# Kernel tuning notes

Measured on AMD Instinct MI355X. Metric: run time of the kernel, lower is better.

Reference implementation:

```python
import jax, jax.numpy as jnp
from jax import lax
import numpy as np

T, INPUT, RES, OUT = 4096, 64, 4096, 32
SPECTRAL_RADIUS, CONNECTIVITY = 0.9, 0.3


def setup_inputs() -> dict:
    key = jax.random.key(0)
    k_in, k_w, k_mask, k_x, k_out = jax.random.split(key, 5)
    inputs = jax.random.normal(k_x, (T, INPUT), dtype=jnp.float32)
    # W_in, W ~ U(-1, 1), as in (rand - 0.5) * 2
    W_in = jax.random.uniform(k_in, (RES, INPUT), minval=-1.0, maxval=1.0, dtype=jnp.float32)
    W = jax.random.uniform(k_w, (RES, RES), minval=-1.0, maxval=1.0, dtype=jnp.float32)
    mask = (jax.random.uniform(k_mask, (RES, RES)) < CONNECTIVITY).astype(jnp.float32)
    W = W * mask
    # rescale to spectral radius (done once at init; numpy eig on host)
    max_eig = np.max(np.abs(np.linalg.eigvals(np.asarray(W))))
    W = W / jnp.float32(max_eig / SPECTRAL_RADIUS)
    # trained readout (stand-in for pinv-solved W_out)
    W_out = jax.random.normal(k_out, (RES, OUT), dtype=jnp.float32) * 0.05
    return {"inputs": inputs, "W_in": W_in, "W": W, "W_out": W_out}


def reference(inputs, W_in, W, W_out):
    # X[:, 0] = 0; X[:, t] = tanh(W_in @ inputs[t] + W @ X[:, t-1]) for t >= 1
    u = inputs @ W_in.T  # [T, RES] precomputed input projections

    def step(x_prev, u_t):
        x_t = jnp.tanh(u_t + W @ x_prev)
        return x_t, x_t

    x0 = jnp.zeros((RES,), dtype=inputs.dtype)
    _, xs = lax.scan(step, x0, u[1:])  # [T-1, RES]
    X = jnp.concatenate([x0[None, :], xs], axis=0)  # [T, RES] == original X.T
    return X @ W_out  # [T, OUT]
```

## Files before the change

kernel.cpp:

```cpp
#include <hip/hip_runtime.h>

#define T_STEPS 4096
#define RES     4096
#define NIN     64
#define NOUT    32
#define NWG     256
#define TPB     512

typedef unsigned long long ull;

__device__ __forceinline__ bool rdy(ull q) {
    return (__uint_as_float((unsigned)q) > 0.5f) &&
           (__uint_as_float((unsigned)(q >> 32)) > 0.5f);
}

__global__ void esn_init(float* __restrict__ Xf) {
    int i = blockIdx.x * 256 + threadIdx.x;
    if (i < RES) Xf[i] = 2.0f;
}

__global__ __launch_bounds__(TPB, 2)
void esn_recur(const float* __restrict__ inp,
               const float* __restrict__ Win,
               const float* __restrict__ W,
               float* __restrict__ Xf)
{
    const int g    = blockIdx.x;
    const int tid  = threadIdx.x;
    const int wv   = tid >> 6;
    const int lane = tid & 63;
    const int r0   = g * 16 + wv * 2;

    __shared__ float xs[2][RES];

    float w0[64], w1[64];
    {
        const float* Wr0 = W + (size_t)r0 * RES + 4 * lane;
        const float* Wr1 = Wr0 + RES;
#pragma unroll
        for (int c = 0; c < 16; ++c) {
            float4 a = *(const float4*)(Wr0 + 256 * c);
            float4 b = *(const float4*)(Wr1 + 256 * c);
            w0[4*c+0] = a.x; w0[4*c+1] = a.y; w0[4*c+2] = a.z; w0[4*c+3] = a.w;
            w1[4*c+0] = b.x; w1[4*c+1] = b.y; w1[4*c+2] = b.z; w1[4*c+3] = b.w;
        }
    }
#pragma unroll
    for (int j = 0; j < 64; ++j) { asm("" : "+v"(w0[j])); asm("" : "+v"(w1[j])); }

    const float win0 = Win[(size_t)(r0 + 0) * NIN + lane];
    const float win1 = Win[(size_t)(r0 + 1) * NIN + lane];

    float u = inp[NIN + lane];

    for (int t = 1; t < T_STEPS; ++t) {
        const ull* src = (const ull*)(Xf + (size_t)(t - 1) * RES) + tid * 4;
        ull q0 = 0, q1 = 0, q2 = 0, q3 = 0;
        int need = 15;
        do {
            if (need & 1) { q0 = __hip_atomic_load(src + 0, __ATOMIC_RELAXED, __HIP_MEMORY_SCOPE_AGENT); if (rdy(q0)) need &= ~1; }
            if (need & 2) { q1 = __hip_atomic_load(src + 1, __ATOMIC_RELAXED, __HIP_MEMORY_SCOPE_AGENT); if (rdy(q1)) need &= ~2; }
            if (need & 4) { q2 = __hip_atomic_load(src + 2, __ATOMIC_RELAXED, __HIP_MEMORY_SCOPE_AGENT); if (rdy(q2)) need &= ~4; }
            if (need & 8) { q3 = __hip_atomic_load(src + 3, __ATOMIC_RELAXED, __HIP_MEMORY_SCOPE_AGENT); if (rdy(q3)) need &= ~8; }
        } while (need);

        float* dst = &xs[t & 1][tid * 8];
        ((float4*)dst)[0] = make_float4(
            __uint_as_float((unsigned)q0)         - 2.0f,
            __uint_as_float((unsigned)(q0 >> 32)) - 2.0f,
            __uint_as_float((unsigned)q1)         - 2.0f,
            __uint_as_float((unsigned)(q1 >> 32)) - 2.0f);
        ((float4*)dst)[1] = make_float4(
            __uint_as_float((unsigned)q2)         - 2.0f,
            __uint_as_float((unsigned)(q2 >> 32)) - 2.0f,
            __uint_as_float((unsigned)q3)         - 2.0f,
            __uint_as_float((unsigned)(q3 >> 32)) - 2.0f);

        float ucur = u;
        if (t + 1 < T_STEPS) u = inp[(size_t)(t + 1) * NIN + lane];

        __syncthreads();

        float a0 = win0 * ucur, a1 = win1 * ucur;
        const float4* xv = (const float4*)&xs[t & 1][4 * lane];
#pragma unroll
        for (int c = 0; c < 16; ++c) {
            float4 x4 = xv[64 * c];
            a0 += w0[4*c+0]*x4.x + w0[4*c+1]*x4.y + w0[4*c+2]*x4.z + w0[4*c+3]*x4.w;
            a1 += w1[4*c+0]*x4.x + w1[4*c+1]*x4.y + w1[4*c+2]*x4.z + w1[4*c+3]*x4.w;
        }
#pragma unroll
        for (int off = 32; off > 0; off >>= 1) {
            a0 += __shfl_xor(a0, off, 64);
            a1 += __shfl_xor(a1, off, 64);
        }

        if (lane < 2) {
            float s  = lane ? a1 : a0;
            float xn = tanhf(s);
            __hip_atomic_store(Xf + (size_t)t * RES + r0 + lane, xn + 2.0f,
                               __ATOMIC_RELAXED, __HIP_MEMORY_SCOPE_AGENT);
        }
    }
}

__global__ __launch_bounds__(256)
void esn_out(const float* __restrict__ Xf,
             const float* __restrict__ Wout,
             float* __restrict__ out)
{
    __shared__ float xs[2 * RES];
    __shared__ float red[2][8][32];
    const int tid = threadIdx.x;
    const int t0  = blockIdx.x * 2;

    const float4* s4 = (const float4*)(Xf + (size_t)t0 * RES);
    float4*       d4 = (float4*)xs;
    for (int i = tid; i < 2 * RES / 4; i += 256) {
        float4 v = s4[i];
        v.x -= 2.0f; v.y -= 2.0f; v.z -= 2.0f; v.w -= 2.0f;
        d4[i] = v;
    }
    __syncthreads();

    const int o  = tid & 31;
    const int sg = tid >> 5;
    float acc0 = 0.f, acc1 = 0.f;
    const int rbeg = sg * 512;
    for (int r = rbeg; r < rbeg + 512; ++r) {
        float wv = Wout[(size_t)r * NOUT + o];
        acc0 += xs[r] * wv;
        acc1 += xs[RES + r] * wv;
    }
    red[0][sg][o] = acc0;
    red[1][sg][o] = acc1;
    __syncthreads();

    if (tid < 64) {
        const int h = tid >> 5, oo = tid & 31;
        float s = 0.f;
#pragma unroll
        for (int k = 0; k < 8; ++k) s += red[h][k][oo];
        out[(size_t)(t0 + h) * NOUT + oo] = s;
    }
}

extern "C" void kernel_launch(void* const* d_in, const int* in_sizes, int n_in,
                              void* d_out, int out_size, void* d_ws, size_t ws_size,
                              hipStream_t stream)
{
    const float* inputs = (const float*)d_in[0];
    const float* W_in   = (const float*)d_in[1];
    const float* W      = (const float*)d_in[2];
    const float* W_out  = (const float*)d_in[3];
    float* out = (float*)d_out;

    float* Xf = (float*)d_ws;

    hipMemsetAsync(Xf, 0, (size_t)T_STEPS * RES * sizeof(float), stream);
    esn_init<<<dim3((RES + 255) / 256), dim3(256), 0, stream>>>(Xf);

    esn_recur<<<dim3(NWG), dim3(TPB), 0, stream>>>(inputs, W_in, W, Xf);
    esn_out<<<dim3(T_STEPS / 2), dim3(256), 0, stream>>>(Xf, W_out, out);
}
```

Before: 13.05 ms.

## Store recurrent weight slice in LDS as fp16 instead of registers

```diff
diff --git a/kernel.cpp b/kernel.cpp
--- a/kernel.cpp
+++ b/kernel.cpp
@@ -1,4 +1,5 @@
 #include <hip/hip_runtime.h>
+#include <hip/hip_fp16.h>
 
 #define T_STEPS 4096
 #define RES     4096
@@ -25,33 +26,36 @@
                const float* __restrict__ W,
                float* __restrict__ Xf)
 {
+    __shared__ __half Wl[16][RES];
+    __shared__ float  xs[RES];
+
     const int g    = blockIdx.x;
     const int tid  = threadIdx.x;
     const int wv   = tid >> 6;
     const int lane = tid & 63;
     const int r0   = g * 16 + wv * 2;
 
-    __shared__ float xs[2][RES];
-
-    float w0[64], w1[64];
     {
-        const float* Wr0 = W + (size_t)r0 * RES + 4 * lane;
-        const float* Wr1 = Wr0 + RES;
-#pragma unroll
-        for (int c = 0; c < 16; ++c) {
-            float4 a = *(const float4*)(Wr0 + 256 * c);
-            float4 b = *(const float4*)(Wr1 + 256 * c);
-            w0[4*c+0] = a.x; w0[4*c+1] = a.y; w0[4*c+2] = a.z; w0[4*c+3] = a.w;
-            w1[4*c+0] = b.x; w1[4*c+1] = b.y; w1[4*c+2] = b.z; w1[4*c+3] = b.w;
+        const float4* Wg = (const float4*)(W + (size_t)g * 16 * RES);
+        for (int idx = tid; idx < 16 * RES / 4; idx += TPB) {
+            float4 v  = Wg[idx];
+            int  row  = idx >> 10;
+            int  c4   = (idx & 1023) * 4;
+            Wl[row][c4 + 0] = __float2half_rn(v.x);
+            Wl[row][c4 + 1] = __float2half_rn(v.y);
+            Wl[row][c4 + 2] = __float2half_rn(v.z);
+            Wl[row][c4 + 3] = __float2half_rn(v.w);
         }
     }
-#pragma unroll
-    for (int j = 0; j < 64; ++j) { asm("" : "+v"(w0[j])); asm("" : "+v"(w1[j])); }
 
     const float win0 = Win[(size_t)(r0 + 0) * NIN + lane];
     const float win1 = Win[(size_t)(r0 + 1) * NIN + lane];
+    float u = inp[NIN + lane];
 
-    float u = inp[NIN + lane];
+    __syncthreads();
+
+    const __half2* wr0 = (const __half2*)&Wl[2 * wv][0];
+    const __half2* wr1 = (const __half2*)&Wl[2 * wv + 1][0];
 
     for (int t = 1; t < T_STEPS; ++t) {
         const ull* src = (const ull*)(Xf + (size_t)(t - 1) * RES) + tid * 4;
@@ -64,7 +68,9 @@
             if (need & 8) { q3 = __hip_atomic_load(src + 3, __ATOMIC_RELAXED, __HIP_MEMORY_SCOPE_AGENT); if (rdy(q3)) need &= ~8; }
         } while (need);
 
-        float* dst = &xs[t & 1][tid * 8];
+        __syncthreads();
+
+        float* dst = &xs[tid * 8];
         ((float4*)dst)[0] = make_float4(
             __uint_as_float((unsigned)q0)         - 2.0f,
             __uint_as_float((unsigned)(q0 >> 32)) - 2.0f,
@@ -82,12 +88,17 @@
         __syncthreads();
 
         float a0 = win0 * ucur, a1 = win1 * ucur;
-        const float4* xv = (const float4*)&xs[t & 1][4 * lane];
+        const float4* xv = (const float4*)&xs[4 * lane];
 #pragma unroll
         for (int c = 0; c < 16; ++c) {
             float4 x4 = xv[64 * c];
-            a0 += w0[4*c+0]*x4.x + w0[4*c+1]*x4.y + w0[4*c+2]*x4.z + w0[4*c+3]*x4.w;
-            a1 += w1[4*c+0]*x4.x + w1[4*c+1]*x4.y + w1[4*c+2]*x4.z + w1[4*c+3]*x4.w;
+            int cb = 2 * lane + 128 * c;
+            __half2 p0 = wr0[cb], p1 = wr0[cb + 1];
+            __half2 r1 = wr1[cb], r2 = wr1[cb + 1];
+            float2 f0 = __half22float2(p0), f1 = __half22float2(p1);
+            float2 g0 = __half22float2(r1), g1 = __half22float2(r2);
+            a0 += f0.x * x4.x + f0.y * x4.y + f1.x * x4.z + f1.y * x4.w;
+            a1 += g0.x * x4.x + g0.y * x4.y + g1.x * x4.z + g1.y * x4.w;
         }
 #pragma unroll
         for (int off = 32; off > 0; off >>= 1) {
```

Result: slower. 19.15 ms (+46.8%).
